# Kernel optimization log

Measured on AMD Instinct MI355X. Metric: run time of the kernel, lower is better.

## Reference

```python
import jax, jax.numpy as jnp
import numpy as np

D_MODEL = 1024
NUM_HEADS = 16
D_K = D_MODEL // NUM_HEADS


def setup_inputs() -> dict:
    key = jax.random.key(0)
    ks = jax.random.split(key, 9)
    s = 1.0 / np.sqrt(D_MODEL)
    inp = {"x": jax.random.normal(ks[0], (4, 2048, D_MODEL), dtype=jnp.float32)}
    for i, name in enumerate(["q", "k", "v", "o"]):
        inp[f"W_{name}"] = jax.random.uniform(ks[1 + 2 * i], (D_MODEL, D_MODEL), minval=-s, maxval=s, dtype=jnp.float32)
        inp[f"b_{name}"] = jax.random.uniform(ks[2 + 2 * i], (D_MODEL,), minval=-s, maxval=s, dtype=jnp.float32)
    return inp


def reference(x, W_q, b_q, W_k, b_k, W_v, b_v, W_o, b_o):
    B, S, _ = x.shape
    # torch Linear: y = x @ W.T + b ; reshape to [B, H, S, d_k]
    def proj(W, b):
        return (x @ W.T + b).reshape(B, S, NUM_HEADS, D_K).transpose(0, 2, 1, 3)

    Q, K, V = proj(W_q, b_q), proj(W_k, b_k), proj(W_v, b_v)
    scores = jnp.einsum("bhqd,bhkd->bhqk", Q, K) / np.sqrt(D_K).astype(np.float32)
    # additive causal mask: -inf above diagonal
    causal = jnp.triu(jnp.full((S, S), -jnp.inf, dtype=scores.dtype), k=1)
    scores = scores + causal
    attn = jax.nn.softmax(scores, axis=-1)
    attn = jnp.nan_to_num(attn, nan=0.0)
    # dropout is identity in eval mode
    out = jnp.einsum("bhqk,bhkd->bhqd", attn, V)
    out = out.transpose(0, 2, 1, 3).reshape(B, S, D_MODEL)
    return out @ W_o.T + b_o
```

## Files before the change

### kernel.cpp

```cpp
#include <hip/hip_runtime.h>
#include <hip/hip_bf16.h>
#include <stdint.h>

#define D_MODEL 1024
#define SEQ     2048
#define NH      16
#define DK      64
#define PSTR    72

typedef __bf16 bf16x8 __attribute__((ext_vector_type(8)));
typedef float  f32x4  __attribute__((ext_vector_type(4)));
typedef unsigned short u16;

#define CFENCE() asm volatile("" ::: "memory")

__device__ __forceinline__ u16 f2bf(float f) {
    uint32_t u = __float_as_uint(f);
    u += 0x7FFFu + ((u >> 16) & 1u);
    return (u16)(u >> 16);
}

__device__ __forceinline__ void gl2lds16(const u16* g, u16* l) {
    __builtin_amdgcn_global_load_lds(
        (const __attribute__((address_space(1))) uint32_t*)g,
        (__attribute__((address_space(3))) uint32_t*)l, 16, 0, 0);
}

__global__ __launch_bounds__(256) void cvt_kernel(const float* __restrict__ src,
                                                  u16* __restrict__ dst, int n4) {
    int i = blockIdx.x * blockDim.x + threadIdx.x;
    if (i >= n4) return;
    float4 v = reinterpret_cast<const float4*>(src)[i];
    ushort4 o;
    o.x = f2bf(v.x); o.y = f2bf(v.y); o.z = f2bf(v.z); o.w = f2bf(v.w);
    reinterpret_cast<ushort4*>(dst)[i] = o;
}

__global__ __launch_bounds__(256) void cvt4_kernel(
    const float* __restrict__ s0, const float* __restrict__ s1,
    const float* __restrict__ s2, const float* __restrict__ s3,
    u16* __restrict__ d0, u16* __restrict__ d1,
    u16* __restrict__ d2, u16* __restrict__ d3, int n4) {
    int z = blockIdx.y;
    const float* s = (z == 0) ? s0 : (z == 1) ? s1 : (z == 2) ? s2 : s3;
    u16* d = (z == 0) ? d0 : (z == 1) ? d1 : (z == 2) ? d2 : d3;
    int i = blockIdx.x * blockDim.x + threadIdx.x;
    if (i >= n4) return;
    float4 v = reinterpret_cast<const float4*>(s)[i];
    ushort4 o;
    o.x = f2bf(v.x); o.y = f2bf(v.y); o.z = f2bf(v.z); o.w = f2bf(v.w);
    reinterpret_cast<ushort4*>(d)[i] = o;
}

__device__ __forceinline__ void gemm128_body(const u16* __restrict__ Ag,
                                             const u16* __restrict__ Bg,
                                             u16* As, u16* Bs, f32x4 acc[4][4]) {
    const int K = D_MODEL;
    int tid = threadIdx.x, wave = tid >> 6, lane = tid & 63;
    int l15 = lane & 15, quad = lane >> 4;
    int srow = lane >> 2;
    int scol = (lane & 3) * 8;
    int arg4 = (wave >> 1) * 4;
    int brg4 = (wave & 1) * 4;
#pragma unroll 1
    for (int kc = 0; kc < K; kc += 64) {
        __syncthreads();
#pragma unroll
        for (int j = 0; j < 4; ++j) {
            int p = wave * 4 + j;
            int rg = p >> 1, h = p & 1;
            int row = rg * 16 + srow;
            int col = kc + h * 32 + scol;
            gl2lds16(Ag + row * K + col, As + p * 512);
            gl2lds16(Bg + row * K + col, Bs + p * 512);
        }
        __syncthreads();
#pragma unroll
        for (int h = 0; h < 2; ++h) {
            bf16x8 af[4], bfr[4];
#pragma unroll
            for (int s = 0; s < 4; ++s) {
                af[s]  = *reinterpret_cast<const bf16x8*>(
                    As + ((arg4 + s) * 2 + h) * 512 + l15 * 32 + quad * 8);
                bfr[s] = *reinterpret_cast<const bf16x8*>(
                    Bs + ((brg4 + s) * 2 + h) * 512 + l15 * 32 + quad * 8);
            }
#pragma unroll
            for (int ms = 0; ms < 4; ++ms)
#pragma unroll
                for (int ns = 0; ns < 4; ++ns)
                    acc[ms][ns] = __builtin_amdgcn_mfma_f32_16x16x32_bf16(
                        af[ms], bfr[ns], acc[ms][ns], 0, 0, 0);
        }
    }
}

__device__ __forceinline__ void stage_half(const u16* __restrict__ gb, u16* ls,
                                           int w2, int srow, int scol) {
#pragma unroll
    for (int i = 0; i < 2; ++i)
        gl2lds16(gb + ((w2 + i) * 8 + srow) * D_MODEL + scol,
                 ls + (w2 + i) * 512);
}

__global__ __launch_bounds__(512, 2) void qkv_gemm256(
    const u16* __restrict__ xb,
    const u16* __restrict__ Wq, const u16* __restrict__ Wk, const u16* __restrict__ Wv,
    const float* __restrict__ bq, const float* __restrict__ bk, const float* __restrict__ bv,
    u16* __restrict__ qo, u16* __restrict__ ko, u16* __restrict__ vto) {
    __shared__ __align__(16) u16 smA[2][2][8192];
    __shared__ __align__(16) u16 smB[2][2][8192];
    int z = blockIdx.z;
    const u16* W = (z == 0) ? Wq : (z == 1) ? Wk : Wv;
    const float* bias = (z == 0) ? bq : (z == 1) ? bk : bv;
    int tid = threadIdx.x;
    int lane = tid & 63, wave = tid >> 6;
    int l15 = lane & 15, quad = lane >> 4;
    int wr = wave >> 2, wc = wave & 3;
    int w2 = wave * 2;
    const u16* Abase = xb + (size_t)blockIdx.x * 256 * D_MODEL;
    const u16* Bbase = W + (size_t)blockIdx.y * 256 * D_MODEL;

    int srow = lane >> 3;
    int scol = ((lane & 7) ^ (lane >> 3)) * 8;
    int xb_ = (l15 & 7) << 4;
    int c0 = ((quad * 16) ^ xb_) >> 1;
    int c1 = ((64 + quad * 16) ^ xb_) >> 1;
    int rb0 = (wc & 1) * 64;

    f32x4 acc[8][4];
#pragma unroll
    for (int m = 0; m < 8; ++m)
#pragma unroll
        for (int n = 0; n < 4; ++n) acc[m][n] = (f32x4){0.f, 0.f, 0.f, 0.f};

    stage_half(Abase, &smA[0][0][0], w2, srow, scol);
    stage_half(Abase + 128 * D_MODEL, &smA[0][1][0], w2, srow, scol);
    stage_half(Bbase, &smB[0][0][0], w2, srow, scol);
    stage_half(Bbase + 128 * D_MODEL, &smB[0][1][0], w2, srow, scol);
    stage_half(Abase + 64, &smA[1][0][0], w2, srow, scol);
    asm volatile("s_waitcnt vmcnt(2)" ::: "memory");
    __builtin_amdgcn_s_barrier();
    CFENCE();

#pragma unroll 1
    for (int t = 0; t < 16; ++t) {
        const int p = t & 1;
        const u16* As = &smA[p][wr][0];
        const u16* Bs = &smB[p][wc >> 1][0];
        bf16x8 af[4][2], bfr[4][2];

#pragma unroll
        for (int m = 0; m < 4; ++m) {
            af[m][0] = *reinterpret_cast<const bf16x8*>(As + (m * 16 + l15) * 64 + c0);
            af[m][1] = *reinterpret_cast<const bf16x8*>(As + (m * 16 + l15) * 64 + c1);
        }
#pragma unroll
        for (int nn = 0; nn < 2; ++nn) {
            bfr[nn][0] = *reinterpret_cast<const bf16x8*>(Bs + (rb0 + nn * 16 + l15) * 64 + c0);
            bfr[nn][1] = *reinterpret_cast<const bf16x8*>(Bs + (rb0 + nn * 16 + l15) * 64 + c1);
        }
        if (t < 15) stage_half(Abase + 128 * D_MODEL + (t + 1) * 64,
                               &smA[(t + 1) & 1][1][0], w2, srow, scol);
        CFENCE(); __builtin_amdgcn_s_barrier(); CFENCE();
        __builtin_amdgcn_s_setprio(1);
#pragma unroll
        for (int m = 0; m < 4; ++m)
#pragma unroll
            for (int nn = 0; nn < 2; ++nn) {
                acc[m][nn] = __builtin_amdgcn_mfma_f32_16x16x32_bf16(af[m][0], bfr[nn][0], acc[m][nn], 0, 0, 0);
                acc[m][nn] = __builtin_amdgcn_mfma_f32_16x16x32_bf16(af[m][1], bfr[nn][1], acc[m][nn], 0, 0, 0);
            }
        __builtin_amdgcn_s_setprio(0);
        CFENCE(); __builtin_amdgcn_s_barrier(); CFENCE();

#pragma unroll
        for (int nn = 0; nn < 2; ++nn) {
            bfr[2 + nn][0] = *reinterpret_cast<const bf16x8*>(Bs + (rb0 + (2 + nn) * 16 + l15) * 64 + c0);
            bfr[2 + nn][1] = *reinterpret_cast<const bf16x8*>(Bs + (rb0 + (2 + nn) * 16 + l15) * 64 + c1);
        }
        if (t < 15) stage_half(Bbase + (t + 1) * 64,
                               &smB[(t + 1) & 1][0][0], w2, srow, scol);
        CFENCE(); __builtin_amdgcn_s_barrier(); CFENCE();
        __builtin_amdgcn_s_setprio(1);
#pragma unroll
        for (int m = 0; m < 4; ++m)
#pragma unroll
            for (int nn = 0; nn < 2; ++nn) {
                acc[m][2 + nn] = __builtin_amdgcn_mfma_f32_16x16x32_bf16(af[m][0], bfr[2 + nn][0], acc[m][2 + nn], 0, 0, 0);
                acc[m][2 + nn] = __builtin_amdgcn_mfma_f32_16x16x32_bf16(af[m][1], bfr[2 + nn][1], acc[m][2 + nn], 0, 0, 0);
            }
        __builtin_amdgcn_s_setprio(0);
        CFENCE(); __builtin_amdgcn_s_barrier(); CFENCE();

#pragma unroll
        for (int m = 0; m < 4; ++m) {
            af[m][0] = *reinterpret_cast<const bf16x8*>(As + ((m + 4) * 16 + l15) * 64 + c0);
            af[m][1] = *reinterpret_cast<const bf16x8*>(As + ((m + 4) * 16 + l15) * 64 + c1);
        }
        if (t < 15) stage_half(Bbase + 128 * D_MODEL + (t + 1) * 64,
                               &smB[(t + 1) & 1][1][0], w2, srow, scol);
        CFENCE(); __builtin_amdgcn_s_barrier(); CFENCE();
        __builtin_amdgcn_s_setprio(1);
#pragma unroll
        for (int m = 0; m < 4; ++m)
#pragma unroll
            for (int nn = 0; nn < 2; ++nn) {
                acc[4 + m][nn] = __builtin_amdgcn_mfma_f32_16x16x32_bf16(af[m][0], bfr[nn][0], acc[4 + m][nn], 0, 0, 0);
                acc[4 + m][nn] = __builtin_amdgcn_mfma_f32_16x16x32_bf16(af[m][1], bfr[nn][1], acc[4 + m][nn], 0, 0, 0);
            }
        __builtin_amdgcn_s_setprio(0);
        CFENCE(); __builtin_amdgcn_s_barrier(); CFENCE();

        if (t < 14) stage_half(Abase + (t + 2) * 64,
                               &smA[p][0][0], w2, srow, scol);
        CFENCE(); __builtin_amdgcn_s_barrier(); CFENCE();
        __builtin_amdgcn_s_setprio(1);
#pragma unroll
        for (int m = 0; m < 4; ++m)
#pragma unroll
            for (int nn = 0; nn < 2; ++nn) {
                acc[4 + m][2 + nn] = __builtin_amdgcn_mfma_f32_16x16x32_bf16(af[m][0], bfr[2 + nn][0], acc[4 + m][2 + nn], 0, 0, 0);
                acc[4 + m][2 + nn] = __builtin_amdgcn_mfma_f32_16x16x32_bf16(af[m][1], bfr[2 + nn][1], acc[4 + m][2 + nn], 0, 0, 0);
            }
        __builtin_amdgcn_s_setprio(0);
        if (t < 14) {
            asm volatile("s_waitcnt vmcnt(2)" ::: "memory");
            __builtin_amdgcn_s_barrier(); CFENCE();
        } else if (t == 14) {
            asm volatile("s_waitcnt vmcnt(0)" ::: "memory");
            __builtin_amdgcn_s_barrier(); CFENCE();
        }
    }

    int mw = blockIdx.x * 256 + wr * 128;
    int nwb = blockIdx.y * 256 + wc * 64;
    int hq = (nwb >> 6) & (NH - 1);
    const float qscale = 0.125f * 1.4426950408889634f;

    if (z != 2) {
        u16* dst = (z == 0) ? qo : ko;
        float sc = (z == 0) ? qscale : 1.0f;
        u16* tw = &smA[0][0][0] + wave * 1152;
        float bv0 = bias[nwb + 0 * 16 + l15];
        float bv1 = bias[nwb + 1 * 16 + l15];
        float bv2 = bias[nwb + 2 * 16 + l15];
        float bv3 = bias[nwb + 3 * 16 + l15];
#pragma unroll
        for (int mf = 0; mf < 8; ++mf) {
#pragma unroll
            for (int nf = 0; nf < 4; ++nf) {
                int c = nf * 16 + l15;
                float bv_ = (nf == 0) ? bv0 : (nf == 1) ? bv1 : (nf == 2) ? bv2 : bv3;
#pragma unroll
                for (int r = 0; r < 4; ++r) {
                    int w = quad * 4 + r;
                    tw[w * 72 + (((c >> 3) ^ (w & 7)) << 3) + (c & 7)] =
                        f2bf((acc[mf][nf][r] + bv_) * sc);
                }
            }
            asm volatile("s_waitcnt lgkmcnt(0)" ::: "memory");
#pragma unroll
            for (int i = 0; i < 2; ++i) {
                int w = i * 8 + (lane >> 3);
                bf16x8 vv = *reinterpret_cast<const bf16x8*>(
                    tw + w * 72 + (((lane & 7) ^ (w & 7)) << 3));
                int sg = mw + mf * 16 + w;
                int b = sg >> 11, ss = sg & (SEQ - 1);
                *reinterpret_cast<bf16x8*>(
                    &dst[((b * NH + hq) * SEQ + ss) * DK + (lane & 7) * 8]) = vv;
            }
            asm volatile("s_waitcnt lgkmcnt(0)" ::: "memory");
        }
    } else {
        u16* tw = &smA[0][0][0] + wave * 4608;
        float bv0 = bias[nwb + 0 * 16 + l15];
        float bv1 = bias[nwb + 1 * 16 + l15];
        float bv2 = bias[nwb + 2 * 16 + l15];
        float bv3 = bias[nwb + 3 * 16 + l15];
#pragma unroll
        for (int half = 0; half < 2; ++half) {
#pragma unroll
            for (int mfi = 0; mfi < 4; ++mfi) {
                int mf = half * 4 + mfi;
#pragma unroll
                for (int nf = 0; nf < 4; ++nf) {
                    int w = nf * 16 + l15;
                    float bv_ = (nf == 0) ? bv0 : (nf == 1) ? bv1 : (nf == 2) ? bv2 : bv3;
                    int sl = mfi * 16 + quad * 4;
                    ushort4 pk;
                    pk.x = f2bf(acc[mf][nf][0] + bv_);
                    pk.y = f2bf(acc[mf][nf][1] + bv_);
                    pk.z = f2bf(acc[mf][nf][2] + bv_);
                    pk.w = f2bf(acc[mf][nf][3] + bv_);
                    *reinterpret_cast<ushort4*>(
                        tw + w * 72 + (((sl >> 3) ^ (w & 7)) << 3) + (sl & 7)) = pk;
                }
            }
            asm volatile("s_waitcnt lgkmcnt(0)" ::: "memory");
#pragma unroll
            for (int i = 0; i < 8; ++i) {
                int w = i * 8 + (lane >> 3);
                bf16x8 vv = *reinterpret_cast<const bf16x8*>(
                    tw + w * 72 + (((lane & 7) ^ (w & 7)) << 3));
                int sg = mw + half * 64 + (lane & 7) * 8;
                int b = sg >> 11, ss = sg & (SEQ - 1);
                *reinterpret_cast<bf16x8*>(
                    &vto[((b * NH + hq) * DK + w) * SEQ + ss]) = vv;
            }
            asm volatile("s_waitcnt lgkmcnt(0)" ::: "memory");
        }
    }
}

__global__ __launch_bounds__(256) void out_gemm(
    const u16* __restrict__ ab, const u16* __restrict__ Wo,
    const float* __restrict__ bo, float* __restrict__ out) {
    __shared__ __align__(16) u16 As[16 * 512], Bs[16 * 512];
    int lane = threadIdx.x & 63, wave = threadIdx.x >> 6;
    int l15 = lane & 15, quad = lane >> 4;
    int mw = blockIdx.x * 128 + (wave >> 1) * 64;
    int nw = blockIdx.y * 128 + (wave & 1) * 64;

    f32x4 acc[4][4];
#pragma unroll
    for (int ms = 0; ms < 4; ++ms)
#pragma unroll
        for (int ns = 0; ns < 4; ++ns)
            acc[ms][ns] = (f32x4){0.f, 0.f, 0.f, 0.f};

    gemm128_body(ab + blockIdx.x * 128 * D_MODEL, Wo + blockIdx.y * 128 * D_MODEL,
                 As, Bs, acc);

#pragma unroll
    for (int ns = 0; ns < 4; ++ns) {
        int n = nw + ns * 16 + l15;
        float bv_ = bo[n];
#pragma unroll
        for (int ms = 0; ms < 4; ++ms) {
            int mbase = mw + ms * 16 + quad * 4;
#pragma unroll
            for (int r = 0; r < 4; ++r)
                out[(mbase + r) * D_MODEL + n] = acc[ms][ns][r] + bv_;
        }
    }
}

__global__ __launch_bounds__(256, 2) void attn_kernel(
    const u16* __restrict__ Q, const u16* __restrict__ Kc,
    const u16* __restrict__ Vt, u16* __restrict__ ao) {
    __shared__ __align__(16) u16 Ks[8 * 512], Vs[8 * 512], Plds[4][32 * PSTR];
    int pair = blockIdx.x, bh = blockIdx.y;
    int lane = threadIdx.x & 63, wave = threadIdx.x >> 6;
    int l15 = lane & 15, quad = lane >> 4;
    const u16* Qb = Q + bh * (SEQ * DK);
    const u16* Kb = Kc + bh * (SEQ * DK);
    const u16* Vb = Vt + bh * (DK * SEQ);
    int b = bh >> 4, hh = bh & 15;
    u16* Pw = &Plds[wave][0];

#pragma unroll 1
    for (int ti = 0; ti < 2; ++ti) {
        int t = ti ? (15 - pair) : pair;
        int q0w = t * 128 + wave * 32;
        int qmax = q0w + 31;

        bf16x8 qf[2][2];
#pragma unroll
        for (int nf = 0; nf < 2; ++nf)
#pragma unroll
            for (int h = 0; h < 2; ++h)
                qf[nf][h] = *reinterpret_cast<const bf16x8*>(
                    Qb + (q0w + nf * 16 + l15) * DK + h * 32 + quad * 8);

        f32x4 o[2][4];
#pragma unroll
        for (int ma = 0; ma < 2; ++ma)
#pragma unroll
            for (int nf = 0; nf < 4; ++nf)
                o[ma][nf] = (f32x4){0.f, 0.f, 0.f, 0.f};
        float lsum[2] = {0.f, 0.f};

        int nch = 2 * t + 2;
#pragma unroll 1
        for (int c = 0; c < nch; ++c) {
            int k0 = c * 64;
            __syncthreads();
#pragma unroll
            for (int h = 0; h < 2; ++h) {
                gl2lds16(Kb + (k0 + wave * 16 + l15) * DK + h * 32 + quad * 8,
                         Ks + (wave * 2 + h) * 512);
                gl2lds16(Vb + (wave * 16 + l15) * SEQ + k0 + h * 32 + quad * 8,
                         Vs + (wave * 2 + h) * 512);
            }
            __syncthreads();
            if (k0 > qmax) continue;

            f32x4 s[4][2];
#pragma unroll
            for (int mf = 0; mf < 4; ++mf) {
                bf16x8 kf0 = *reinterpret_cast<const bf16x8*>(Ks + (mf * 2 + 0) * 512 + lane * 8);
                bf16x8 kf1 = *reinterpret_cast<const bf16x8*>(Ks + (mf * 2 + 1) * 512 + lane * 8);
#pragma unroll
                for (int nf = 0; nf < 2; ++nf) {
                    f32x4 z = (f32x4){0.f, 0.f, 0.f, 0.f};
                    z = __builtin_amdgcn_mfma_f32_16x16x32_bf16(kf0, qf[nf][0], z, 0, 0, 0);
                    z = __builtin_amdgcn_mfma_f32_16x16x32_bf16(kf1, qf[nf][1], z, 0, 0, 0);
                    s[mf][nf] = z;
                }
            }
            if (k0 + 63 > q0w) {
#pragma unroll
                for (int mf = 0; mf < 4; ++mf) {
                    int key = k0 + mf * 16 + quad * 4;
#pragma unroll
                    for (int nf = 0; nf < 2; ++nf) {
                        int q = q0w + nf * 16 + l15;
#pragma unroll
                        for (int r = 0; r < 4; ++r)
                            if (key + r > q) s[mf][nf][r] = -__builtin_inff();
                    }
                }
            }
#pragma unroll
            for (int mf = 0; mf < 4; ++mf)
#pragma unroll
                for (int nf = 0; nf < 2; ++nf) {
                    float p0 = __builtin_amdgcn_exp2f(s[mf][nf][0]);
                    float p1 = __builtin_amdgcn_exp2f(s[mf][nf][1]);
                    float p2 = __builtin_amdgcn_exp2f(s[mf][nf][2]);
                    float p3 = __builtin_amdgcn_exp2f(s[mf][nf][3]);
                    lsum[nf] += (p0 + p1) + (p2 + p3);
                    ushort4 pk;
                    pk.x = f2bf(p0); pk.y = f2bf(p1); pk.z = f2bf(p2); pk.w = f2bf(p3);
                    *reinterpret_cast<ushort4*>(
                        Pw + (nf * 16 + l15) * PSTR + mf * 16 + quad * 4) = pk;
                }
            __asm__ volatile("s_waitcnt lgkmcnt(0)" ::: "memory");
            bf16x8 pa[2][2];
#pragma unroll
            for (int ma = 0; ma < 2; ++ma)
#pragma unroll
                for (int h = 0; h < 2; ++h)
                    pa[ma][h] = *reinterpret_cast<const bf16x8*>(
                        Pw + (ma * 16 + l15) * PSTR + h * 32 + quad * 8);
#pragma unroll
            for (int nf = 0; nf < 4; ++nf) {
                bf16x8 vf0 = *reinterpret_cast<const bf16x8*>(Vs + (nf * 2 + 0) * 512 + lane * 8);
                bf16x8 vf1 = *reinterpret_cast<const bf16x8*>(Vs + (nf * 2 + 1) * 512 + lane * 8);
#pragma unroll
                for (int ma = 0; ma < 2; ++ma) {
                    o[ma][nf] = __builtin_amdgcn_mfma_f32_16x16x32_bf16(pa[ma][0], vf0, o[ma][nf], 0, 0, 0);
                    o[ma][nf] = __builtin_amdgcn_mfma_f32_16x16x32_bf16(pa[ma][1], vf1, o[ma][nf], 0, 0, 0);
                }
            }
        }
        lsum[0] += __shfl_xor(lsum[0], 16);
        lsum[0] += __shfl_xor(lsum[0], 32);
        lsum[1] += __shfl_xor(lsum[1], 16);
        lsum[1] += __shfl_xor(lsum[1], 32);
#pragma unroll
        for (int ma = 0; ma < 2; ++ma) {
#pragma unroll
            for (int r = 0; r < 4; ++r) {
                float inv = __builtin_amdgcn_rcpf(__shfl(lsum[ma], quad * 4 + r));
                int q = q0w + ma * 16 + quad * 4 + r;
#pragma unroll
                for (int nf = 0; nf < 4; ++nf) {
                    int d = nf * 16 + l15;
                    ao[(b * SEQ + q) * D_MODEL + hh * DK + d] = f2bf(o[ma][nf][r] * inv);
                }
            }
        }
    }
}

extern "C" void kernel_launch(void* const* d_in, const int* in_sizes, int n_in,
                              void* d_out, int out_size, void* d_ws, size_t ws_size,
                              hipStream_t stream) {
    const float* x  = (const float*)d_in[0];
    const float* Wq = (const float*)d_in[1];
    const float* bq = (const float*)d_in[2];
    const float* Wk = (const float*)d_in[3];
    const float* bk = (const float*)d_in[4];
    const float* Wv = (const float*)d_in[5];
    const float* bv = (const float*)d_in[6];
    const float* Wo = (const float*)d_in[7];
    const float* bo = (const float*)d_in[8];
    float* out = (float*)d_out;
    char* ws = (char*)d_ws;

    const size_t XB = 16777216;
    const size_t WB = 2097152;
    u16* xb  = (u16*)(ws);
    u16* wqb = (u16*)(ws + XB);
    u16* wkb = (u16*)(ws + XB + WB);
    u16* wvb = (u16*)(ws + XB + 2 * WB);
    u16* wob = (u16*)(ws + XB + 3 * WB);
    u16* qb  = (u16*)(ws + XB + 4 * WB);
    u16* kb  = (u16*)(ws + 2 * XB + 4 * WB);
    u16* vtb = (u16*)(ws + 3 * XB + 4 * WB);
    u16* ab  = (u16*)(ws + 4 * XB + 4 * WB);

    cvt_kernel<<<8192, 256, 0, stream>>>(x, xb, 2097152);
    cvt4_kernel<<<dim3(1024, 4), 256, 0, stream>>>(Wq, Wk, Wv, Wo,
                                                   wqb, wkb, wvb, wob, 262144);

    qkv_gemm256<<<dim3(32, 4, 3), 512, 0, stream>>>(xb, wqb, wkb, wvb, bq, bk, bv,
                                                    qb, kb, vtb);
    attn_kernel<<<dim3(8, 64), 256, 0, stream>>>(qb, kb, vtb, ab);
    out_gemm<<<dim3(64, 8), 256, 0, stream>>>(ab, wob, bo, out);
}
```

Measured before the change: 269.8 us.

## Double-buffer K/V tiles in attention and give each block one query tile

```diff
diff --git a/kernel.cpp b/kernel.cpp
--- a/kernel.cpp
+++ b/kernel.cpp
@@ -346,11 +346,11 @@
     }
 }
 
-__global__ __launch_bounds__(256, 2) void attn_kernel(
+__global__ __launch_bounds__(256, 3) void attn_kernel(
     const u16* __restrict__ Q, const u16* __restrict__ Kc,
     const u16* __restrict__ Vt, u16* __restrict__ ao) {
-    __shared__ __align__(16) u16 Ks[8 * 512], Vs[8 * 512], Plds[4][32 * PSTR];
-    int pair = blockIdx.x, bh = blockIdx.y;
+    __shared__ __align__(16) u16 Ks[2][8 * 512], Vs[2][8 * 512], Plds[4][32 * PSTR];
+    int t = 15 - blockIdx.x, bh = blockIdx.y;
     int lane = threadIdx.x & 63, wave = threadIdx.x >> 6;
     int l15 = lane & 15, quad = lane >> 4;
     const u16* Qb = Q + bh * (SEQ * DK);
@@ -359,117 +359,132 @@
     int b = bh >> 4, hh = bh & 15;
     u16* Pw = &Plds[wave][0];
 
+    int q0w = t * 128 + wave * 32;
+    int qmax = q0w + 31;
+
+    bf16x8 qf[2][2];
+#pragma unroll
+    for (int nf = 0; nf < 2; ++nf)
+#pragma unroll
+        for (int h = 0; h < 2; ++h)
+            qf[nf][h] = *reinterpret_cast<const bf16x8*>(
+                Qb + (q0w + nf * 16 + l15) * DK + h * 32 + quad * 8);
+
+    f32x4 o[2][4];
+#pragma unroll
+    for (int ma = 0; ma < 2; ++ma)
+#pragma unroll
+        for (int nf = 0; nf < 4; ++nf)
+            o[ma][nf] = (f32x4){0.f, 0.f, 0.f, 0.f};
+    float lsum[2] = {0.f, 0.f};
+
+    int nch = 2 * t + 2;
+
+#pragma unroll
+    for (int h = 0; h < 2; ++h) {
+        gl2lds16(Kb + (wave * 16 + l15) * DK + h * 32 + quad * 8,
+                 &Ks[0][(wave * 2 + h) * 512]);
+        gl2lds16(Vb + (wave * 16 + l15) * SEQ + h * 32 + quad * 8,
+                 &Vs[0][(wave * 2 + h) * 512]);
+    }
+
 #pragma unroll 1
-    for (int ti = 0; ti < 2; ++ti) {
-        int t = ti ? (15 - pair) : pair;
-        int q0w = t * 128 + wave * 32;
-        int qmax = q0w + 31;
-
-        bf16x8 qf[2][2];
-#pragma unroll
-        for (int nf = 0; nf < 2; ++nf)
+    for (int c = 0; c < nch; ++c) {
+        int k0 = c * 64;
+        int cur = c & 1;
+        CFENCE(); __builtin_amdgcn_s_barrier(); CFENCE();
+        if (c + 1 < nch) {
+            int k1 = k0 + 64;
+#pragma unroll
+            for (int h = 0; h < 2; ++h) {
+                gl2lds16(Kb + (k1 + wave * 16 + l15) * DK + h * 32 + quad * 8,
+                         &Ks[cur ^ 1][(wave * 2 + h) * 512]);
+                gl2lds16(Vb + (wave * 16 + l15) * SEQ + k1 + h * 32 + quad * 8,
+                         &Vs[cur ^ 1][(wave * 2 + h) * 512]);
+            }
+            asm volatile("s_waitcnt vmcnt(4)" ::: "memory");
+        } else {
+            asm volatile("s_waitcnt vmcnt(0)" ::: "memory");
+        }
+        CFENCE(); __builtin_amdgcn_s_barrier(); CFENCE();
+        if (k0 > qmax) continue;
+
+        const u16* Kcur = &Ks[cur][0];
+        const u16* Vcur = &Vs[cur][0];
+
+        f32x4 s[4][2];
+#pragma unroll
+        for (int mf = 0; mf < 4; ++mf) {
+            bf16x8 kf0 = *reinterpret_cast<const bf16x8*>(Kcur + (mf * 2 + 0) * 512 + lane * 8);
+            bf16x8 kf1 = *reinterpret_cast<const bf16x8*>(Kcur + (mf * 2 + 1) * 512 + lane * 8);
+#pragma unroll
+            for (int nf = 0; nf < 2; ++nf) {
+                f32x4 z = (f32x4){0.f, 0.f, 0.f, 0.f};
+                z = __builtin_amdgcn_mfma_f32_16x16x32_bf16(kf0, qf[nf][0], z, 0, 0, 0);
+                z = __builtin_amdgcn_mfma_f32_16x16x32_bf16(kf1, qf[nf][1], z, 0, 0, 0);
+                s[mf][nf] = z;
+            }
+        }
+        if (k0 + 63 > q0w) {
+#pragma unroll
+            for (int mf = 0; mf < 4; ++mf) {
+                int key = k0 + mf * 16 + quad * 4;
+#pragma unroll
+                for (int nf = 0; nf < 2; ++nf) {
+                    int q = q0w + nf * 16 + l15;
+#pragma unroll
+                    for (int r = 0; r < 4; ++r)
+                        if (key + r > q) s[mf][nf][r] = -__builtin_inff();
+                }
+            }
+        }
+#pragma unroll
+        for (int mf = 0; mf < 4; ++mf)
+#pragma unroll
+            for (int nf = 0; nf < 2; ++nf) {
+                float p0 = __builtin_amdgcn_exp2f(s[mf][nf][0]);
+                float p1 = __builtin_amdgcn_exp2f(s[mf][nf][1]);
+                float p2 = __builtin_amdgcn_exp2f(s[mf][nf][2]);
+                float p3 = __builtin_amdgcn_exp2f(s[mf][nf][3]);
+                lsum[nf] += (p0 + p1) + (p2 + p3);
+                ushort4 pk;
+                pk.x = f2bf(p0); pk.y = f2bf(p1); pk.z = f2bf(p2); pk.w = f2bf(p3);
+                *reinterpret_cast<ushort4*>(
+                    Pw + (nf * 16 + l15) * PSTR + mf * 16 + quad * 4) = pk;
+            }
+        __asm__ volatile("s_waitcnt lgkmcnt(0)" ::: "memory");
+        bf16x8 pa[2][2];
+#pragma unroll
+        for (int ma = 0; ma < 2; ++ma)
 #pragma unroll
             for (int h = 0; h < 2; ++h)
-                qf[nf][h] = *reinterpret_cast<const bf16x8*>(
-                    Qb + (q0w + nf * 16 + l15) * DK + h * 32 + quad * 8);
-
-        f32x4 o[2][4];
-#pragma unroll
-        for (int ma = 0; ma < 2; ++ma)
-#pragma unroll
-            for (int nf = 0; nf < 4; ++nf)
-                o[ma][nf] = (f32x4){0.f, 0.f, 0.f, 0.f};
-        float lsum[2] = {0.f, 0.f};
-
-        int nch = 2 * t + 2;
-#pragma unroll 1
-        for (int c = 0; c < nch; ++c) {
-            int k0 = c * 64;
-            __syncthreads();
-#pragma unroll
-            for (int h = 0; h < 2; ++h) {
-                gl2lds16(Kb + (k0 + wave * 16 + l15) * DK + h * 32 + quad * 8,
-                         Ks + (wave * 2 + h) * 512);
-                gl2lds16(Vb + (wave * 16 + l15) * SEQ + k0 + h * 32 + quad * 8,
-                         Vs + (wave * 2 + h) * 512);
-            }
-            __syncthreads();
-            if (k0 > qmax) continue;
-
-            f32x4 s[4][2];
-#pragma unroll
-            for (int mf = 0; mf < 4; ++mf) {
-                bf16x8 kf0 = *reinterpret_cast<const bf16x8*>(Ks + (mf * 2 + 0) * 512 + lane * 8);
-                bf16x8 kf1 = *reinterpret_cast<const bf16x8*>(Ks + (mf * 2 + 1) * 512 + lane * 8);
-#pragma unroll
-                for (int nf = 0; nf < 2; ++nf) {
-                    f32x4 z = (f32x4){0.f, 0.f, 0.f, 0.f};
-                    z = __builtin_amdgcn_mfma_f32_16x16x32_bf16(kf0, qf[nf][0], z, 0, 0, 0);
-                    z = __builtin_amdgcn_mfma_f32_16x16x32_bf16(kf1, qf[nf][1], z, 0, 0, 0);
-                    s[mf][nf] = z;
-                }
-            }
-            if (k0 + 63 > q0w) {
-#pragma unroll
-                for (int mf = 0; mf < 4; ++mf) {
-                    int key = k0 + mf * 16 + quad * 4;
-#pragma unroll
-                    for (int nf = 0; nf < 2; ++nf) {
-                        int q = q0w + nf * 16 + l15;
-#pragma unroll
-                        for (int r = 0; r < 4; ++r)
-                            if (key + r > q) s[mf][nf][r] = -__builtin_inff();
-                    }
-                }
-            }
-#pragma unroll
-            for (int mf = 0; mf < 4; ++mf)
-#pragma unroll
-                for (int nf = 0; nf < 2; ++nf) {
-                    float p0 = __builtin_amdgcn_exp2f(s[mf][nf][0]);
-                    float p1 = __builtin_amdgcn_exp2f(s[mf][nf][1]);
-                    float p2 = __builtin_amdgcn_exp2f(s[mf][nf][2]);
-                    float p3 = __builtin_amdgcn_exp2f(s[mf][nf][3]);
-                    lsum[nf] += (p0 + p1) + (p2 + p3);
-                    ushort4 pk;
-                    pk.x = f2bf(p0); pk.y = f2bf(p1); pk.z = f2bf(p2); pk.w = f2bf(p3);
-                    *reinterpret_cast<ushort4*>(
-                        Pw + (nf * 16 + l15) * PSTR + mf * 16 + quad * 4) = pk;
-                }
-            __asm__ volatile("s_waitcnt lgkmcnt(0)" ::: "memory");
-            bf16x8 pa[2][2];
-#pragma unroll
-            for (int ma = 0; ma < 2; ++ma)
-#pragma unroll
-                for (int h = 0; h < 2; ++h)
-                    pa[ma][h] = *reinterpret_cast<const bf16x8*>(
-                        Pw + (ma * 16 + l15) * PSTR + h * 32 + quad * 8);
+                pa[ma][h] = *reinterpret_cast<const bf16x8*>(
+                    Pw + (ma * 16 + l15) * PSTR + h * 32 + quad * 8);
+#pragma unroll
+        for (int nf = 0; nf < 4; ++nf) {
+            bf16x8 vf0 = *reinterpret_cast<const bf16x8*>(Vcur + (nf * 2 + 0) * 512 + lane * 8);
+            bf16x8 vf1 = *reinterpret_cast<const bf16x8*>(Vcur + (nf * 2 + 1) * 512 + lane * 8);
+#pragma unroll
+            for (int ma = 0; ma < 2; ++ma) {
+                o[ma][nf] = __builtin_amdgcn_mfma_f32_16x16x32_bf16(pa[ma][0], vf0, o[ma][nf], 0, 0, 0);
+                o[ma][nf] = __builtin_amdgcn_mfma_f32_16x16x32_bf16(pa[ma][1], vf1, o[ma][nf], 0, 0, 0);
+            }
+        }
+    }
+    lsum[0] += __shfl_xor(lsum[0], 16);
+    lsum[0] += __shfl_xor(lsum[0], 32);
+    lsum[1] += __shfl_xor(lsum[1], 16);
+    lsum[1] += __shfl_xor(lsum[1], 32);
+#pragma unroll
+    for (int ma = 0; ma < 2; ++ma) {
+#pragma unroll
+        for (int r = 0; r < 4; ++r) {
+            float inv = __builtin_amdgcn_rcpf(__shfl(lsum[ma], quad * 4 + r));
+            int q = q0w + ma * 16 + quad * 4 + r;
 #pragma unroll
             for (int nf = 0; nf < 4; ++nf) {
-                bf16x8 vf0 = *reinterpret_cast<const bf16x8*>(Vs + (nf * 2 + 0) * 512 + lane * 8);
-                bf16x8 vf1 = *reinterpret_cast<const bf16x8*>(Vs + (nf * 2 + 1) * 512 + lane * 8);
-#pragma unroll
-                for (int ma = 0; ma < 2; ++ma) {
-                    o[ma][nf] = __builtin_amdgcn_mfma_f32_16x16x32_bf16(pa[ma][0], vf0, o[ma][nf], 0, 0, 0);
-                    o[ma][nf] = __builtin_amdgcn_mfma_f32_16x16x32_bf16(pa[ma][1], vf1, o[ma][nf], 0, 0, 0);
-                }
-            }
-        }
-        lsum[0] += __shfl_xor(lsum[0], 16);
-        lsum[0] += __shfl_xor(lsum[0], 32);
-        lsum[1] += __shfl_xor(lsum[1], 16);
-        lsum[1] += __shfl_xor(lsum[1], 32);
-#pragma unroll
-        for (int ma = 0; ma < 2; ++ma) {
-#pragma unroll
-            for (int r = 0; r < 4; ++r) {
-                float inv = __builtin_amdgcn_rcpf(__shfl(lsum[ma], quad * 4 + r));
-                int q = q0w + ma * 16 + quad * 4 + r;
-#pragma unroll
-                for (int nf = 0; nf < 4; ++nf) {
-                    int d = nf * 16 + l15;
-                    ao[(b * SEQ + q) * D_MODEL + hh * DK + d] = f2bf(o[ma][nf][r] * inv);
-                }
+                int d = nf * 16 + l15;
+                ao[(b * SEQ + q) * D_MODEL + hh * DK + d] = f2bf(o[ma][nf][r] * inv);
             }
         }
     }
@@ -508,6 +523,6 @@
 
     qkv_gemm256<<<dim3(32, 4, 3), 512, 0, stream>>>(xb, wqb, wkb, wvb, bq, bk, bv,
                                                     qb, kb, vtb);
-    attn_kernel<<<dim3(8, 64), 256, 0, stream>>>(qb, kb, vtb, ab);
+    attn_kernel<<<dim3(16, 64), 256, 0, stream>>>(qb, kb, vtb, ab);
     out_gemm<<<dim3(64, 8), 256, 0, stream>>>(ab, wob, bo, out);
 }
```

Measured after the change: 308.9 us. +14.5%, slower.
